# Kernel optimization log

Hardware: AMD Instinct MI355X
Metric: run time of the kernel (lower is better)

Reference implementation:

```python
import jax, jax.numpy as jnp
import numpy as np

N = 4096
E = 262144
IN_DIM = 256
EDGE_DIM = 16
NUM_ATOM_FEATURES = 16
LATENT_DIM = 128
NUM_BOND_TYPES = 5


def setup_inputs() -> dict:
    key = jax.random.key(0)
    ks = jax.random.split(key, 12)
    inp = {
        's': jax.random.normal(ks[0], (N, IN_DIM), dtype=jnp.float32),
        'e': jax.random.normal(ks[1], (E, EDGE_DIM), dtype=jnp.float32),
        'batch': jnp.zeros((N,), dtype=jnp.int64),
        'edge_index_global': jax.random.randint(ks[2], (2, E), 0, N, dtype=jnp.int64),
        # learned parameters (torch nn.Linear layout: W is [out, in])
        'W_shared': jax.random.normal(ks[3], (IN_DIM, IN_DIM), dtype=jnp.float32) * 0.02,
        'b_shared': jnp.zeros((IN_DIM,), dtype=jnp.float32),
        'W_bond': jax.random.normal(ks[4], (IN_DIM, EDGE_DIM), dtype=jnp.float32) * 0.02,
        'b_bond': jnp.zeros((IN_DIM,), dtype=jnp.float32),
        'W_bonds': jax.random.normal(ks[5], (NUM_BOND_TYPES, IN_DIM), dtype=jnp.float32) * 0.02,
        'b_bonds': jnp.zeros((NUM_BOND_TYPES,), dtype=jnp.float32),
        'W_atoms': jax.random.normal(ks[6], (NUM_ATOM_FEATURES + LATENT_DIM, IN_DIM), dtype=jnp.float32) * 0.02,
        'b_atoms': jnp.zeros((NUM_ATOM_FEATURES + LATENT_DIM,), dtype=jnp.float32),
    }
    return inp


def reference(s, e, batch, edge_index_global,
              W_shared, b_shared, W_bond, b_bond,
              W_bonds, b_bonds, W_atoms, b_atoms):
    # shared_mapping: Linear + SiLU
    s = jax.nn.silu(s @ W_shared.T + b_shared)  # [n, in_dim]
    j = edge_index_global[0]
    i = edge_index_global[1]
    n = s.shape[0]

    # atoms_lin then split into atom-type logits and latent prediction
    atoms_out = s @ W_atoms.T + b_atoms  # [n, num_atom_features + latent_dim]
    atoms_pred = atoms_out[:, :NUM_ATOM_FEATURES]
    latent_pred = atoms_out[:, NUM_ATOM_FEATURES:]

    # dense scatter -> symmetrize -> gather (faithful to the original O(n^2) path)
    e_dense = jnp.zeros((n, n, e.shape[-1]), dtype=e.dtype).at[j, i].set(e)
    e_dense = 0.5 * (e_dense + e_dense.transpose(1, 0, 2))
    e_sym = e_dense[j, i]  # [E, edge_dim]

    # fused gather + bond linear + SiLU + bonds linear
    f = jax.nn.silu(s[i] + s[j] + e_sym @ W_bond.T + b_bond)  # [E, in_dim]
    bonds_pred = f @ W_bonds.T + b_bonds  # [E, num_bond_types]

    return (latent_pred, atoms_pred, bonds_pred)
```

## Files before the change

### kernel.cpp

```cpp
#include <hip/hip_runtime.h>
#include <hip/hip_bf16.h>

#define N_NODES   4096
#define E_EDGES   262144
#define IN_DIM    256
#define EDGE_DIM  16
#define NAF       16
#define LATENT    128
#define NBT       5

#define LATENT_OFF 0
#define ATOMS_OFF  (N_NODES * LATENT)
#define BONDS_OFF  (ATOMS_OFF + N_NODES * NAF)

#define TBITS 20
#define TSIZE (1u << TBITS)
#define TMASK (TSIZE - 1u)

typedef float    f32x4  __attribute__((ext_vector_type(4)));
typedef float    f32x4v __attribute__((ext_vector_type(4)));
typedef short    bf16x8 __attribute__((ext_vector_type(8)));
typedef unsigned u32x2  __attribute__((ext_vector_type(2)));
typedef unsigned u32x4  __attribute__((ext_vector_type(4)));

__device__ __forceinline__ float silu_f(float x) {
    return x * __builtin_amdgcn_rcpf(1.0f + __expf(-x));
}

__device__ __forceinline__ unsigned pack_bf16x2(float lo, float hi) {
#if __has_builtin(__builtin_amdgcn_cvt_pk_bf16_f32)
    typedef __bf16 bf16x2_t __attribute__((ext_vector_type(2)));
    union { bf16x2_t v; unsigned u; } c;
    c.v = __builtin_amdgcn_cvt_pk_bf16_f32(lo, hi);
    return c.u;
#else
    union { float f; unsigned u; } a, b;
    a.f = lo; b.f = hi;
    const unsigned ra = (a.u + 0x7FFFu + ((a.u >> 16) & 1u)) >> 16;
    const unsigned rb = (b.u + 0x7FFFu + ((b.u >> 16) & 1u)) >> 16;
    return ra | (rb << 16);
#endif
}

__device__ __forceinline__ float bf_lo(unsigned u) {
    union { unsigned x; float f; } c; c.x = u << 16; return c.f;
}
__device__ __forceinline__ float bf_hi(unsigned u) {
    union { unsigned x; float f; } c; c.x = u & 0xFFFF0000u; return c.f;
}

__device__ __forceinline__ void split_bf16(const float4 x0, const float4 x1,
                                           bf16x8* hi, bf16x8* lo) {
    union { bf16x8 v; unsigned u[4]; } H, L;
    H.u[0] = pack_bf16x2(x0.x, x0.y);
    H.u[1] = pack_bf16x2(x0.z, x0.w);
    H.u[2] = pack_bf16x2(x1.x, x1.y);
    H.u[3] = pack_bf16x2(x1.z, x1.w);
    L.u[0] = pack_bf16x2(x0.x - bf_lo(H.u[0]), x0.y - bf_hi(H.u[0]));
    L.u[1] = pack_bf16x2(x0.z - bf_lo(H.u[1]), x0.w - bf_hi(H.u[1]));
    L.u[2] = pack_bf16x2(x1.x - bf_lo(H.u[2]), x1.y - bf_hi(H.u[2]));
    L.u[3] = pack_bf16x2(x1.z - bf_lo(H.u[3]), x1.w - bf_hi(H.u[3]));
    *hi = H.v; *lo = L.v;
}

__device__ __forceinline__ void gld_lds16(const void* g, void* l) {
    __builtin_amdgcn_global_load_lds(
        (const __attribute__((address_space(1))) unsigned*)g,
        (__attribute__((address_space(3))) unsigned*)l, 16, 0, 0);
}

__device__ __forceinline__ unsigned hashh(unsigned key) {
    return (key * 2654435761u) >> (32 - TBITS);
}

__device__ __forceinline__ int resolve2(const unsigned long long* __restrict__ tab,
                                        unsigned key, unsigned long long s0,
                                        unsigned long long s1, unsigned h) {
    if ((unsigned)(s0 >> 18) == key + 1u) return (int)(s0 & 0x3FFFFu);
    if (s0 == 0ULL) return -1;
    if ((unsigned)(s1 >> 18) == key + 1u) return (int)(s1 & 0x3FFFFu);
    if (s1 == 0ULL) return -1;
    h = (h + 2u) & TMASK;
    while (true) {
        const unsigned long long cur = tab[h];
        if (cur == 0ULL) return -1;
        if ((unsigned)(cur >> 18) == key + 1u) return (int)(cur & 0x3FFFFu);
        h = (h + 1u) & TMASK;
    }
}

__global__ __launch_bounds__(256) void k_front(const float* __restrict__ s,
                                               const float* __restrict__ Wsh,
                                               const float* __restrict__ bsh,
                                               const int* __restrict__ eidx,
                                               const float* __restrict__ Wb,
                                               const float* __restrict__ bb,
                                               const float* __restrict__ Wbs,
                                               unsigned short* __restrict__ sact16,
                                               unsigned long long* __restrict__ tab,
                                               u32x4* __restrict__ A1pre,
                                               u32x4* __restrict__ A2pre) {
    __shared__ short sWh[32][264];
    __shared__ short sWl[32][264];

    const int blk = blockIdx.x;
    const int c   = threadIdx.x;

    if (blk >= 512) {
        if (blk < 1536) {
            const int k = (blk - 512) * 256 + c;
            const unsigned j = (unsigned)eidx[k];
            const unsigned i = (unsigned)eidx[E_EDGES + k];
            const unsigned key = (j << 12) | i;
            const unsigned long long mine =
                ((unsigned long long)(key + 1u) << 18) | (unsigned)k;
            unsigned h = hashh(key);
            while (true) {
                const unsigned long long old = atomicCAS(&tab[h], 0ULL, mine);
                if (old == 0ULL) return;
                if ((unsigned)(old >> 18) == key + 1u) {
                    atomicMax(&tab[h], mine);
                    return;
                }
                h = (h + 1u) & TMASK;
            }
        } else {
#pragma unroll
            for (int ee = 0; ee < 4; ++ee) {
                const int idx  = c + 256 * ee;
                const int g    = idx >> 6;
                const int lane = idx & 63;
                const int mm   = lane & 15;
                const int qq   = lane >> 4;

                const float4 w = *(const float4*)(Wb + (16 * g + mm) * EDGE_DIM + 4 * qq);
                u32x4 r1;
                r1.x = pack_bf16x2(w.x, w.y);
                r1.y = pack_bf16x2(w.z, w.w);
                r1.z = pack_bf16x2(bb[16 * g + mm], 0.0f);
                r1.w = 0u;
                A1pre[idx] = r1;

                u32x4 r2;
                if (mm < NBT) {
                    const float4 ws = *(const float4*)(Wbs + mm * IN_DIM + 16 * g + 4 * qq);
                    r2.x = pack_bf16x2(ws.x, ws.y);
                    r2.y = pack_bf16x2(ws.z, ws.w);
                } else {
                    r2.x = 0u; r2.y = 0u;
                }
                r2.z = 0u; r2.w = 0u;
                A2pre[idx] = r2;
            }
        }
        return;
    }

    const int rg = blk >> 3;
    const int cg = blk & 7;

    {
        const int r  = c >> 3;
        const int cq = c & 7;
        const float* wrow = Wsh + (size_t)(cg * 32 + r) * IN_DIM;
#pragma unroll
        for (int k = 0; k < 4; ++k) {
            const int ch = cq + 8 * k;
            const float4 b0 = *(const float4*)(wrow + ch * 8);
            const float4 b1 = *(const float4*)(wrow + ch * 8 + 4);
            bf16x8 Bh, Bl;
            split_bf16(b0, b1, &Bh, &Bl);
            *(bf16x8*)&sWh[r][ch * 8] = Bh;
            *(bf16x8*)&sWl[r][ch * 8] = Bl;
        }
    }
    __syncthreads();

    const int lane = c & 63;
    const int wv   = c >> 6;
    const int m    = lane & 15;
    const int q    = lane >> 4;
    const int row0 = rg * 64 + wv * 16;

    f32x4v acc0, acc1;
    {
        const float b0 = bsh[cg * 32 + m];
        const float b1 = bsh[cg * 32 + 16 + m];
        acc0[0] = b0; acc0[1] = b0; acc0[2] = b0; acc0[3] = b0;
        acc1[0] = b1; acc1[1] = b1; acc1[2] = b1; acc1[3] = b1;
    }

    const float* ap = s + (size_t)(row0 + m) * IN_DIM + 8 * q;

#pragma unroll
    for (int c8 = 0; c8 < 8; ++c8) {
        const float4 a0 = *(const float4*)(ap + 32 * c8);
        const float4 a1 = *(const float4*)(ap + 32 * c8 + 4);
        bf16x8 Ah, Al;
        split_bf16(a0, a1, &Ah, &Al);

        {
            const bf16x8 Bh = *(const bf16x8*)&sWh[m][32 * c8 + 8 * q];
            const bf16x8 Bl = *(const bf16x8*)&sWl[m][32 * c8 + 8 * q];
            acc0 = __builtin_amdgcn_mfma_f32_16x16x32_bf16(Ah, Bh, acc0, 0, 0, 0);
            acc0 = __builtin_amdgcn_mfma_f32_16x16x32_bf16(Al, Bh, acc0, 0, 0, 0);
            acc0 = __builtin_amdgcn_mfma_f32_16x16x32_bf16(Ah, Bl, acc0, 0, 0, 0);
        }
        {
            const bf16x8 Bh = *(const bf16x8*)&sWh[16 + m][32 * c8 + 8 * q];
            const bf16x8 Bl = *(const bf16x8*)&sWl[16 + m][32 * c8 + 8 * q];
            acc1 = __builtin_amdgcn_mfma_f32_16x16x32_bf16(Ah, Bh, acc1, 0, 0, 0);
            acc1 = __builtin_amdgcn_mfma_f32_16x16x32_bf16(Al, Bh, acc1, 0, 0, 0);
            acc1 = __builtin_amdgcn_mfma_f32_16x16x32_bf16(Ah, Bl, acc1, 0, 0, 0);
        }
    }

#pragma unroll
    for (int r = 0; r < 4; ++r) {
        const int row = row0 + 4 * q + r;
        const float v0 = silu_f(acc0[r]);
        const float v1 = silu_f(acc1[r]);
        sact16[(size_t)row * IN_DIM + cg * 32 + m] =
            (unsigned short)(pack_bf16x2(v0, 0.0f) & 0xFFFFu);
        sact16[(size_t)row * IN_DIM + cg * 32 + 16 + m] =
            (unsigned short)(pack_bf16x2(v1, 0.0f) & 0xFFFFu);
    }
}

#define SB0()    __builtin_amdgcn_sched_barrier(0)
#define LGKM0()  do { __asm__ __volatile__("s_waitcnt lgkmcnt(0)" ::: "memory"); SB0(); } while (0)
#define VMW(n)   do { __asm__ __volatile__("s_waitcnt vmcnt(" #n ")" ::: "memory"); SB0(); } while (0)

__global__ __launch_bounds__(256, 6) void k_edges_mfma(const int* __restrict__ eidx,
                                                       const float* __restrict__ e,
                                                       const unsigned long long* __restrict__ tab,
                                                       const unsigned short* __restrict__ sact16,
                                                       const u32x4* __restrict__ A1pre,
                                                       const u32x4* __restrict__ A2pre,
                                                       const float* __restrict__ bbs,
                                                       const float* __restrict__ Wa,
                                                       const float* __restrict__ ba,
                                                       float* __restrict__ out) {
    __shared__ unsigned lds_all[4][1536];
    const int blk  = blockIdx.x;
    const int lane = threadIdx.x & 63;
    const int wv   = threadIdx.x >> 6;
    const int m    = lane & 15;
    const int q    = lane >> 4;

    if (blk >= 4096) {
        const int wave = (blk - 4096) * 4 + wv;
        const int rt = wave / 9;
        const int ct = wave - rt * 9;
        const int row0  = rt * 16;
        const int n_abs = ct * 16 + m;

        f32x4v acc;
        {
            const float bias = ba[n_abs];
            acc[0] = bias; acc[1] = bias; acc[2] = bias; acc[3] = bias;
        }

        const unsigned short* apu = sact16 + (size_t)(row0 + m) * IN_DIM + 8 * q;
        const float*          bp  = Wa + (size_t)n_abs * IN_DIM + 8 * q;

#pragma unroll
        for (int c8 = 0; c8 < 8; ++c8) {
            const bf16x8 A = *(const bf16x8*)(apu + 32 * c8);
            const float4 b0 = *(const float4*)(bp + 32 * c8);
            const float4 b1 = *(const float4*)(bp + 32 * c8 + 4);
            bf16x8 Bh, Bl;
            split_bf16(b0, b1, &Bh, &Bl);
            acc = __builtin_amdgcn_mfma_f32_16x16x32_bf16(A, Bh, acc, 0, 0, 0);
            acc = __builtin_amdgcn_mfma_f32_16x16x32_bf16(A, Bl, acc, 0, 0, 0);
        }
#pragma unroll
        for (int r = 0; r < 4; ++r) {
            const int row = row0 + 4 * q + r;
            if (n_abs < NAF)
                out[ATOMS_OFF + (size_t)row * NAF + n_abs] = acc[r];
            else
                out[LATENT_OFF + (size_t)row * LATENT + (n_abs - NAF)] = acc[r];
        }
        return;
    }

    const int k0 = __builtin_amdgcn_readfirstlane((blk * 4 + wv) * 16);
    unsigned* myl = lds_all[wv];
    const short one_q0 = (q == 0) ? (short)0x3F80 : (short)0;

    f32x4v acc_init;
#pragma unroll
    for (int r = 0; r < 4; ++r) {
        const int bond = 4 * q + r;
        acc_init[r] = (bond < NBT) ? bbs[bond] : 0.0f;
    }
    const int qh = q >> 1;
    const int qw = 2 * (q & 1);
    const int mw = m * 4;

    const unsigned j_m = (unsigned)eidx[k0 + m];
    const unsigned i_m = (unsigned)eidx[E_EDGES + k0 + m];

    const char* si_base = (const char*)(sact16 + (size_t)i_m * IN_DIM);
    const char* sj_base = (const char*)(sact16 + (size_t)j_m * IN_DIM);

    const unsigned keyF = (j_m << 12) | i_m, keyR = (i_m << 12) | j_m;
    const unsigned hF = hashh(keyF), hR = hashh(keyR);
    const unsigned long long sF0 = tab[hF];
    const unsigned long long sF1 = tab[(hF + 1u) & TMASK];
    const unsigned long long sR0 = tab[hR];
    const unsigned long long sR1 = tab[(hR + 1u) & TMASK];

    auto stage_e = [&](int p, int qb) {
        gld_lds16(si_base + p * 64 + q * 16, (char*)myl + qb);
        gld_lds16(sj_base + p * 64 + q * 16, (char*)myl + qb + 1024);
        SB0();
    };

    stage_e(0, 0);
    stage_e(1, 2048);
    stage_e(2, 4096);

    const int wf = resolve2(tab, keyF, sF0, sF1, hF);
    const int wr = resolve2(tab, keyR, sR0, sR1, hR);

    const float rsc = (wr >= 0) ? 0.5f : 0.0f;
    const int   wrc = (wr >= 0) ? wr : 0;
    const f32x4 ef = *(const f32x4*)(e + (size_t)wf  * EDGE_DIM + 4 * q);
    const f32x4 er = *(const f32x4*)(e + (size_t)wrc * EDGE_DIM + 4 * q);

    union { bf16x8 v; short s[8]; unsigned u[4]; } B1;
    {
        const f32x4 es = ef * 0.5f + er * rsc;
        B1.u[0] = pack_bf16x2(es[0], es[1]);
        B1.u[1] = pack_bf16x2(es[2], es[3]);
        B1.s[4] = one_q0; B1.s[5] = 0;
        B1.u[3] = 0u;
    }

    f32x4v acc0 = acc_init;
    f32x4v acc1 = {0.0f, 0.0f, 0.0f, 0.0f};

    auto qcompute2 = [&](int qb4, int gbase) {
#pragma unroll
        for (int gp = 0; gp < 2; ++gp) {
            const int g   = gbase + gp;
            const int off = (2 * gp + qh) * 64 + mw + qw;

            const u32x2 wi = *(const u32x2*)(myl + qb4 + off);
            const u32x2 wj = *(const u32x2*)(myl + qb4 + 256 + off);

            f32x4v C1;
            C1[0] = bf_lo(wi.x) + bf_lo(wj.x);
            C1[1] = bf_hi(wi.x) + bf_hi(wj.x);
            C1[2] = bf_lo(wi.y) + bf_lo(wj.y);
            C1[3] = bf_hi(wi.y) + bf_hi(wj.y);

            const u32x4 r1 = A1pre[g * 64 + lane];
            const u32x4 r2 = A2pre[g * 64 + lane];
            union { bf16x8 v; unsigned u[4]; } A1, A2;
            A1.u[0] = r1.x; A1.u[1] = r1.y; A1.u[2] = r1.z; A1.u[3] = 0u;
            A2.u[0] = r2.x; A2.u[1] = r2.y; A2.u[2] = 0u;   A2.u[3] = 0u;

            const f32x4v P = __builtin_amdgcn_mfma_f32_16x16x32_bf16(A1.v, B1.v, C1, 0, 0, 0);

            union { bf16x8 v; unsigned u[4]; } B2;
            B2.u[0] = pack_bf16x2(silu_f(P[0]), silu_f(P[1]));
            B2.u[1] = pack_bf16x2(silu_f(P[2]), silu_f(P[3]));
            B2.u[2] = 0u; B2.u[3] = 0u;

            if (gp & 1) acc1 = __builtin_amdgcn_mfma_f32_16x16x32_bf16(A2.v, B2.v, acc1, 0, 0, 0);
            else        acc0 = __builtin_amdgcn_mfma_f32_16x16x32_bf16(A2.v, B2.v, acc0, 0, 0, 0);
        }
    };

    VMW(0);
    qcompute2(0, 0);
    LGKM0(); stage_e(3, 0);

    VMW(2);
    qcompute2(512, 2);
    LGKM0(); stage_e(4, 2048);

    VMW(4);
    qcompute2(1024, 4);
    LGKM0(); stage_e(5, 4096);

    VMW(4);
    qcompute2(0, 6);
    LGKM0(); stage_e(6, 0);

    VMW(4);
    qcompute2(512, 8);
    LGKM0(); stage_e(7, 2048);

    VMW(4);
    qcompute2(1024, 10);

    VMW(2);
    qcompute2(0, 12);

    VMW(0);
    qcompute2(512, 14);

    const f32x4v accT = acc0 + acc1;
    float* op = out + BONDS_OFF + (size_t)(k0 + m) * NBT;
    if (q == 0) {
        op[0] = accT[0];
        op[1] = accT[1];
        op[2] = accT[2];
        op[3] = accT[3];
    } else if (q == 1) {
        op[4] = accT[0];
    }
}

extern "C" void kernel_launch(void* const* d_in, const int* in_sizes, int n_in,
                              void* d_out, int out_size, void* d_ws, size_t ws_size,
                              hipStream_t stream) {
    const float* s   = (const float*)d_in[0];
    const float* e   = (const float*)d_in[1];
    const int*   eix = (const int*)d_in[3];
    const float* Wsh = (const float*)d_in[4];
    const float* bsh = (const float*)d_in[5];
    const float* Wb  = (const float*)d_in[6];
    const float* bbo = (const float*)d_in[7];
    const float* Wbs = (const float*)d_in[8];
    const float* bbs = (const float*)d_in[9];
    const float* Wa  = (const float*)d_in[10];
    const float* ba  = (const float*)d_in[11];
    float* out = (float*)d_out;

    char* ws = (char*)d_ws;
    unsigned short*     sact16 = (unsigned short*)ws;
    u32x4*              A1pre  = (u32x4*)(ws + (2u << 20));
    u32x4*              A2pre  = (u32x4*)(ws + (2u << 20) + 16384);
    unsigned long long* tab    = (unsigned long long*)(ws + (3u << 20));

    (void)hipMemsetAsync(tab, 0x00, TSIZE * sizeof(unsigned long long), stream);

    k_front<<<1537, 256, 0, stream>>>(s, Wsh, bsh, eix, Wb, bbo, Wbs,
                                      sact16, tab, A1pre, A2pre);
    k_edges_mfma<<<4672, 256, 0, stream>>>(eix, e, tab, sact16,
                                           A1pre, A2pre, bbs, Wa, ba, out);
}
```

Before: 172.3 us.

## Cache forward hash slots, sum node gathers via identity MFMA, reorder atom blocks first

The hash insert now records each edge's final table slot, so the edge kernel reads the forward entry directly instead of probing for it. The per-lane bf16 unpack and add of the gathered s[i]+s[j] rows is replaced by two MFMAs with a selector identity matrix, which reads whole 16-byte LDS vectors in a new LDS layout. The atom-linear blocks move to the front of the grid so they start first. This adds two MFMAs per group and a workspace array in exchange for fewer VALU ops and fewer probe loads.

```diff
diff --git a/kernel.cpp b/kernel.cpp
--- a/kernel.cpp
+++ b/kernel.cpp
@@ -99,7 +99,8 @@
                                                unsigned short* __restrict__ sact16,
                                                unsigned long long* __restrict__ tab,
                                                u32x4* __restrict__ A1pre,
-                                               u32x4* __restrict__ A2pre) {
+                                               u32x4* __restrict__ A2pre,
+                                               unsigned* __restrict__ slotk) {
     __shared__ short sWh[32][264];
     __shared__ short sWl[32][264];
 
@@ -117,13 +118,15 @@
             unsigned h = hashh(key);
             while (true) {
                 const unsigned long long old = atomicCAS(&tab[h], 0ULL, mine);
-                if (old == 0ULL) return;
+                if (old == 0ULL) break;
                 if ((unsigned)(old >> 18) == key + 1u) {
                     atomicMax(&tab[h], mine);
-                    return;
+                    break;
                 }
                 h = (h + 1u) & TMASK;
             }
+            slotk[k] = h;
+            return;
         } else {
 #pragma unroll
             for (int ee = 0; ee < 4; ++ee) {
@@ -152,8 +155,8 @@
                 r2.z = 0u; r2.w = 0u;
                 A2pre[idx] = r2;
             }
-        }
-        return;
+            return;
+        }
     }
 
     const int rg = blk >> 3;
@@ -240,6 +243,7 @@
                                                        const float* __restrict__ bbs,
                                                        const float* __restrict__ Wa,
                                                        const float* __restrict__ ba,
+                                                       const unsigned* __restrict__ slotk,
                                                        float* __restrict__ out) {
     __shared__ unsigned lds_all[4][1536];
     const int blk  = blockIdx.x;
@@ -248,8 +252,8 @@
     const int m    = lane & 15;
     const int q    = lane >> 4;
 
-    if (blk >= 4096) {
-        const int wave = (blk - 4096) * 4 + wv;
+    if (blk < 576) {
+        const int wave = blk * 4 + wv;
         const int rt = wave / 9;
         const int ct = wave - rt * 9;
         const int row0  = rt * 16;
@@ -285,7 +289,7 @@
         return;
     }
 
-    const int k0 = __builtin_amdgcn_readfirstlane((blk * 4 + wv) * 16);
+    const int k0 = __builtin_amdgcn_readfirstlane(((blk - 576) * 4 + wv) * 16);
     unsigned* myl = lds_all[wv];
     const short one_q0 = (q == 0) ? (short)0x3F80 : (short)0;
 
@@ -295,9 +299,19 @@
         const int bond = 4 * q + r;
         acc_init[r] = (bond < NBT) ? bbs[bond] : 0.0f;
     }
-    const int qh = q >> 1;
-    const int qw = 2 * (q & 1);
-    const int mw = m * 4;
+
+    union { bf16x8 v; unsigned u[4]; } IA;
+    {
+        const int active = (q == 1 + (m >> 3));
+        const unsigned val = active ? (0x3F80u << (16 * (m & 1))) : 0u;
+        const int widx = (m & 7) >> 1;
+        IA.u[0] = (widx == 0) ? val : 0u;
+        IA.u[1] = (widx == 1) ? val : 0u;
+        IA.u[2] = (widx == 2) ? val : 0u;
+        IA.u[3] = (widx == 3) ? val : 0u;
+    }
+    const f32x4v zeroC = {0.0f, 0.0f, 0.0f, 0.0f};
+    const int soff = 256 * (q >> 1) + 16 * m;
 
     const unsigned j_m = (unsigned)eidx[k0 + m];
     const unsigned i_m = (unsigned)eidx[E_EDGES + k0 + m];
@@ -305,10 +319,10 @@
     const char* si_base = (const char*)(sact16 + (size_t)i_m * IN_DIM);
     const char* sj_base = (const char*)(sact16 + (size_t)j_m * IN_DIM);
 
-    const unsigned keyF = (j_m << 12) | i_m, keyR = (i_m << 12) | j_m;
-    const unsigned hF = hashh(keyF), hR = hashh(keyR);
-    const unsigned long long sF0 = tab[hF];
-    const unsigned long long sF1 = tab[(hF + 1u) & TMASK];
+    const unsigned sl = slotk[k0 + m];
+    const unsigned long long fv = tab[sl];
+    const unsigned keyR = (i_m << 12) | j_m;
+    const unsigned hR = hashh(keyR);
     const unsigned long long sR0 = tab[hR];
     const unsigned long long sR1 = tab[(hR + 1u) & TMASK];
 
@@ -322,7 +336,7 @@
     stage_e(1, 2048);
     stage_e(2, 4096);
 
-    const int wf = resolve2(tab, keyF, sF0, sF1, hF);
+    const int wf = (int)(fv & 0x3FFFFu);
     const int wr = resolve2(tab, keyR, sR0, sR1, hR);
 
     const float rsc = (wr >= 0) ? 0.5f : 0.0f;
@@ -342,20 +356,14 @@
     f32x4v acc0 = acc_init;
     f32x4v acc1 = {0.0f, 0.0f, 0.0f, 0.0f};
 
-    auto qcompute2 = [&](int qb4, int gbase) {
+    auto qcompute2 = [&](int qbB, int gbase) {
 #pragma unroll
         for (int gp = 0; gp < 2; ++gp) {
-            const int g   = gbase + gp;
-            const int off = (2 * gp + qh) * 64 + mw + qw;
-
-            const u32x2 wi = *(const u32x2*)(myl + qb4 + off);
-            const u32x2 wj = *(const u32x2*)(myl + qb4 + 256 + off);
-
-            f32x4v C1;
-            C1[0] = bf_lo(wi.x) + bf_lo(wj.x);
-            C1[1] = bf_hi(wi.x) + bf_hi(wj.x);
-            C1[2] = bf_lo(wi.y) + bf_lo(wj.y);
-            C1[3] = bf_hi(wi.y) + bf_hi(wj.y);
+            const int g    = gbase + gp;
+            const int half = g & 1;
+
+            const bf16x8 SI = *(const bf16x8*)((const char*)myl + qbB + 512 * half + soff);
+            const bf16x8 SJ = *(const bf16x8*)((const char*)myl + qbB + 512 * half + 1024 + soff);
 
             const u32x4 r1 = A1pre[g * 64 + lane];
             const u32x4 r2 = A2pre[g * 64 + lane];
@@ -363,7 +371,9 @@
             A1.u[0] = r1.x; A1.u[1] = r1.y; A1.u[2] = r1.z; A1.u[3] = 0u;
             A2.u[0] = r2.x; A2.u[1] = r2.y; A2.u[2] = 0u;   A2.u[3] = 0u;
 
-            const f32x4v P = __builtin_amdgcn_mfma_f32_16x16x32_bf16(A1.v, B1.v, C1, 0, 0, 0);
+            f32x4v P0 = __builtin_amdgcn_mfma_f32_16x16x32_bf16(IA.v, SI, zeroC, 0, 0, 0);
+            P0 = __builtin_amdgcn_mfma_f32_16x16x32_bf16(IA.v, SJ, P0, 0, 0, 0);
+            const f32x4v P = __builtin_amdgcn_mfma_f32_16x16x32_bf16(A1.v, B1.v, P0, 0, 0, 0);
 
             union { bf16x8 v; unsigned u[4]; } B2;
             B2.u[0] = pack_bf16x2(silu_f(P[0]), silu_f(P[1]));
@@ -380,11 +390,11 @@
     LGKM0(); stage_e(3, 0);
 
     VMW(2);
-    qcompute2(512, 2);
+    qcompute2(2048, 2);
     LGKM0(); stage_e(4, 2048);
 
     VMW(4);
-    qcompute2(1024, 4);
+    qcompute2(4096, 4);
     LGKM0(); stage_e(5, 4096);
 
     VMW(4);
@@ -392,17 +402,17 @@
     LGKM0(); stage_e(6, 0);
 
     VMW(4);
-    qcompute2(512, 8);
+    qcompute2(2048, 8);
     LGKM0(); stage_e(7, 2048);
 
     VMW(4);
-    qcompute2(1024, 10);
+    qcompute2(4096, 10);
 
     VMW(2);
     qcompute2(0, 12);
 
     VMW(0);
-    qcompute2(512, 14);
+    qcompute2(2048, 14);
 
     const f32x4v accT = acc0 + acc1;
     float* op = out + BONDS_OFF + (size_t)(k0 + m) * NBT;
@@ -437,11 +447,12 @@
     u32x4*              A1pre  = (u32x4*)(ws + (2u << 20));
     u32x4*              A2pre  = (u32x4*)(ws + (2u << 20) + 16384);
     unsigned long long* tab    = (unsigned long long*)(ws + (3u << 20));
+    unsigned*           slotk  = (unsigned*)(ws + (11u << 20));
 
     (void)hipMemsetAsync(tab, 0x00, TSIZE * sizeof(unsigned long long), stream);
 
     k_front<<<1537, 256, 0, stream>>>(s, Wsh, bsh, eix, Wb, bbo, Wbs,
-                                      sact16, tab, A1pre, A2pre);
+                                      sact16, tab, A1pre, A2pre, slotk);
     k_edges_mfma<<<4672, 256, 0, stream>>>(eix, e, tab, sact16,
-                                           A1pre, A2pre, bbs, Wa, ba, out);
-}
+                                           A1pre, A2pre, bbs, Wa, ba, slotk, out);
+}
```

New measurement: 169.8 us. No clear change (-1.4%).
